# Kernel tuning notes

Hardware: AMD Instinct MI355X
Metric: run time of the kernel (lower is better)

The kernel has to match this reference:

```python
import jax, jax.numpy as jnp
import numpy as np
from math import factorial

LMAX = 2
C_DIM = 128
N = 50000
# (l1, l2, l_out) 'uuu' (channel-wise, no weights) instructions, as in the module ([:3])
INSTR = [(2, 2, 0), (1, 2, 1), (1, 1, 2)]


def _f(n):
    return float(factorial(int(n)))


def _su2_cg(j1, m1, j2, m2, j3, m3):
    # Clebsch-Gordan <j1 m1 j2 m2 | j3 m3> (Racah formula), complex SU(2) basis
    if m3 != m1 + m2:
        return 0.0
    vmin = int(max(-j1 + j2 + m3, -j1 + m1, 0))
    vmax = int(min(j2 + j3 + m1, j3 - j1 + j2, j3 + m3))
    pref = ((2 * j3 + 1) * _f(j3 + j1 - j2) * _f(j3 - j1 + j2) * _f(j1 + j2 - j3) / _f(j1 + j2 + j3 + 1)
            * _f(j3 + m3) * _f(j3 - m3) / (_f(j1 - m1) * _f(j1 + m1) * _f(j2 - m2) * _f(j2 + m2))) ** 0.5
    s = 0.0
    for v in range(vmin, vmax + 1):
        s += (-1.0) ** (v + j2 + m2) / _f(v) * _f(j2 + j3 + m1 - v) * _f(j1 - m1 + v) / (
            _f(j3 - j1 + j2 - v) * _f(j3 + m3 - v) * _f(v + j1 - j2 - m3))
    return pref * s


def _q_real_to_complex(l):
    # e3nn change-of-basis from real to complex spherical harmonics
    q = np.zeros((2 * l + 1, 2 * l + 1), dtype=np.complex128)
    for m in range(-l, 0):
        q[l + m, l + abs(m)] = 1.0 / np.sqrt(2)
        q[l + m, l - abs(m)] = -1j / np.sqrt(2)
    q[l, l] = 1.0
    for m in range(1, l + 1):
        q[l + m, l + abs(m)] = (-1) ** m / np.sqrt(2)
        q[l + m, l - abs(m)] = 1j * (-1) ** m / np.sqrt(2)
    return (-1j) ** l * q


def wigner_3j(l1, l2, l3):
    # real-basis Wigner 3j, unit Frobenius norm (e3nn convention)
    Csu2 = np.zeros((2 * l1 + 1, 2 * l2 + 1, 2 * l3 + 1), dtype=np.complex128)
    for i, m1 in enumerate(range(-l1, l1 + 1)):
        for k, m2 in enumerate(range(-l2, l2 + 1)):
            for n, m3 in enumerate(range(-l3, l3 + 1)):
                Csu2[i, k, n] = _su2_cg(l1, m1, l2, m2, l3, m3)
    Q1, Q2, Q3 = _q_real_to_complex(l1), _q_real_to_complex(l2), _q_real_to_complex(l3)
    C = np.einsum('ij,kl,mn,ikn->jlm', Q1, Q2, np.conj(Q3.T), Csu2)
    assert np.abs(C.imag).max() < 1e-7
    C = C.real
    return (C / np.linalg.norm(C)).astype(np.float32)


W3J = {(l1, l2, lo): jnp.asarray(wigner_3j(l1, l2, lo)) for (l1, l2, lo) in INSTR}


def so3_linear(x, W, b):
    # per-degree block-diagonal linear; x: [N, (LMAX+1)^2, Cin], W: [LMAX+1, Cout, Cin], b: [Cout] (l=0 only)
    outs = []
    for l in range(LMAX + 1):
        y = jnp.einsum('nmc,dc->nmd', x[:, l * l:(l + 1) * (l + 1), :], W[l])
        if l == 0:
            y = y + b
        outs.append(y)
    return jnp.concatenate(outs, axis=1)


def tensor_product_uuu(x1, x2):
    # sparse CG tensor product, channel-shared ('uuu'), no path weights
    out = jnp.zeros_like(x1)
    for (l1, l2, lo) in INSTR:
        w3j = W3J[(l1, l2, lo)]
        alpha = float((2 * lo + 1) ** 0.5)  # component normalization
        blk = alpha * jnp.einsum('ijk,nic,njc->nkc', w3j,
                                 x1[:, l1 * l1:(l1 + 1) ** 2, :],
                                 x2[:, l2 * l2:(l2 + 1) ** 2, :])
        out = out.at[:, lo * lo:(lo + 1) ** 2, :].add(blk)
    return out


def setup_inputs() -> dict:
    key = jax.random.key(0)
    ks = jax.random.split(key, 7)
    scale = 1.0 / np.sqrt(C_DIM)
    m_dim = (LMAX + 1) ** 2  # 9
    return {
        'irreps_x': jax.random.normal(ks[0], (N, m_dim, C_DIM), jnp.float32),
        'W_left': jax.random.normal(ks[1], (LMAX + 1, C_DIM, C_DIM), jnp.float32) * scale,
        'b_left': jax.random.normal(ks[2], (C_DIM,), jnp.float32) * scale,
        'W_right': jax.random.normal(ks[3], (LMAX + 1, C_DIM, C_DIM), jnp.float32) * scale,
        'b_right': jax.random.normal(ks[4], (C_DIM,), jnp.float32) * scale,
        'W_final': jax.random.normal(ks[5], (LMAX + 1, C_DIM, C_DIM), jnp.float32) * scale,
        'b_final': jax.random.normal(ks[6], (C_DIM,), jnp.float32) * scale,
    }


def reference(irreps_x, W_left, b_left, W_right, b_right, W_final, b_final):
    xl = so3_linear(irreps_x, W_left, b_left)
    xr = so3_linear(irreps_x, W_right, b_right)
    out = tensor_product_uuu(xl, xr)
    return so3_linear(out, W_final, b_final)  # [N, 9, C]
```

## Files before the change

kernel.cpp:

```cpp
#include <hip/hip_runtime.h>
#include <cmath>
#include <complex>

typedef unsigned short u16;
typedef unsigned int u32;
typedef __bf16 bf16x8 __attribute__((ext_vector_type(8)));
typedef __bf16 bf16x2 __attribute__((ext_vector_type(2)));
typedef float f32x4 __attribute__((ext_vector_type(4)));
typedef float f32x2 __attribute__((ext_vector_type(2)));

#define CD 128
#define TILE_N 8
#define XS 136
#define LS 132

#define SMEM_TOTAL (72 * XS + 64 * LS + 64 * LS)

struct TPW { float w220[25]; float w121[45]; float w112[45]; };

__device__ __forceinline__ u32 pk2(float a, float b) {
  bf16x2 h;
  h.x = (__bf16)a;
  h.y = (__bf16)b;
  return __builtin_bit_cast(u32, h);
}
__device__ __forceinline__ f32x2 unpk(u32 v) {
  f32x2 r;
  r.x = __uint_as_float(v << 16);
  r.y = __uint_as_float(v & 0xffff0000u);
  return r;
}

__device__ __forceinline__ void ldw4(uint4* dst, const u16* base) {
#pragma unroll
  for (int kk = 0; kk < 4; ++kk)
    dst[kk] = *(const uint4*)(base + kk * 32);
}

__device__ __forceinline__ f32x4 mf(const uint4& a, const uint4& b, f32x4 c) {
  return __builtin_amdgcn_mfma_f32_16x16x32_bf16(
      __builtin_bit_cast(bf16x8, a), __builtin_bit_cast(bf16x8, b), c, 0, 0, 0);
}

__device__ __forceinline__ void stA(u16* d, const f32x4& a) {
  u32 p01 = pk2(a[0], a[1]);
  u32 p23 = pk2(a[2], a[3]);
  d[0]      = (u16)p01;
  d[LS]     = (u16)(p01 >> 16);
  d[2 * LS] = (u16)p23;
  d[3 * LS] = (u16)(p23 >> 16);
}

__global__ void cvt_weights_kernel(const float* __restrict__ Wl,
                                   const float* __restrict__ Wr,
                                   const float* __restrict__ Wf,
                                   u16* __restrict__ ws) {
  int idx = (blockIdx.x * 256 + threadIdx.x) * 8;
  const float* src; int off;
  if (idx < 49152)      { src = Wl; off = idx; }
  else if (idx < 98304) { src = Wr; off = idx - 49152; }
  else                  { src = Wf; off = idx - 98304; }
  float4 a = *(const float4*)(src + off);
  float4 b = *(const float4*)(src + off + 4);
  uint4 v;
  v.x = pk2(a.x, a.y);
  v.y = pk2(a.z, a.w);
  v.z = pk2(b.x, b.y);
  v.w = pk2(b.z, b.w);
  *(uint4*)(ws + idx) = v;
}

__global__ __launch_bounds__(256, 3)
void fused_kernel(const float* __restrict__ x, const u16* __restrict__ ws,
                  const float* __restrict__ bfin, float* __restrict__ out,
                  int N, TPW tw) {
  __shared__ __align__(16) u16 smem[SMEM_TOTAL];
  u16* bufX = smem;
  u16* sTP  = smem;
  u16* sL   = smem + 72 * XS;
  u16* sR   = smem + 72 * XS + 64 * LS;

  const int tid  = threadIdx.x;
  const int n0   = blockIdx.x * TILE_N;
  const int w    = tid >> 6;
  const int lane = tid & 63;
  const int q    = lane >> 4;
  const int lr   = lane & 15;

  const int mat = w >> 1;
  const int wl  = w & 1;
  u16* dstA = mat ? sR : sL;
  const u16* wsA = ws + mat * 3 * 16384;
  const u16* wsf = ws + 6 * 16384;

  const int dc0 = w * 16 + lr;
  const int dc1 = dc0 + 64;
  const float bias0 = bfin[dc0];
  const float bias1 = bfin[dc1];

#pragma unroll
  for (int it = 0; it < 4; ++it) {
    int e = (it * 256 + tid) * 8;
    int r = e >> 7;
    int c = e & 127;
    int n = n0 + (r & 7);
    if (n >= N) n = N - 1;
    int grow = (n * 9 + 1 + (r >> 3)) * CD + c;
    float4 a = *(const float4*)(x + grow);
    float4 b = *(const float4*)(x + grow + 4);
    uint4 v;
    v.x = pk2(a.x, a.y);
    v.y = pk2(a.z, a.w);
    v.z = pk2(b.x, b.y);
    v.w = pk2(b.z, b.w);
    *(uint4*)(bufX + r * XS + c) = v;
  }

  uint4 bfA[4], bfB[4];
  {
    const int colA0 = wl * 64 + lr;
    ldw4(bfA, wsA + 16384 + colA0 * CD + q * 8);
    ldw4(bfB, wsA + 16384 + (colA0 + 16) * CD + q * 8);
  }
  __syncthreads();

#pragma unroll
  for (int p = 0; p < 2; ++p) {
    const int colA = wl * 64 + p * 32 + lr;
    const int colB = colA + 16;
    if (p == 1) {
      ldw4(bfA, wsA + 16384 + colA * CD + q * 8);
      ldw4(bfB, wsA + 16384 + colB * CD + q * 8);
    }
#pragma unroll
    for (int rt = 0; rt < 2; ++rt) {
      const int gbase = rt * 16;
      int ga = gbase + lr; if (ga > 23) ga = 23;
      uint4 av[4];
      ldw4(av, bufX + ga * XS + q * 8);
      f32x4 accA = {0.f, 0.f, 0.f, 0.f};
      f32x4 accB = {0.f, 0.f, 0.f, 0.f};
#pragma unroll
      for (int kk = 0; kk < 4; ++kk) {
        accA = mf(av[kk], bfA[kk], accA);
        accB = mf(av[kk], bfB[kk], accB);
      }
      int g0 = gbase + q * 4;
      if (g0 < 24) {
        stA(dstA + g0 * LS + colA, accA);
        stA(dstA + g0 * LS + colB, accB);
      }
    }
    ldw4(bfA, wsA + 2 * 16384 + colA * CD + q * 8);
    ldw4(bfB, wsA + 2 * 16384 + colB * CD + q * 8);
#pragma unroll
    for (int rt = 0; rt < 3; ++rt) {
      const int gbase = rt * 16;
      int ga = gbase + lr; if (ga > 39) ga = 39;
      uint4 av[4];
      ldw4(av, bufX + (24 + ga) * XS + q * 8);
      f32x4 accA = {0.f, 0.f, 0.f, 0.f};
      f32x4 accB = {0.f, 0.f, 0.f, 0.f};
#pragma unroll
      for (int kk = 0; kk < 4; ++kk) {
        accA = mf(av[kk], bfA[kk], accA);
        accB = mf(av[kk], bfB[kk], accB);
      }
      int g0 = gbase + q * 4;
      if (g0 < 40) {
        stA(dstA + (24 + g0) * LS + colA, accA);
        stA(dstA + (24 + g0) * LS + colB, accB);
      }
    }
  }
  __syncthreads();

#pragma unroll
  for (int iter = 0; iter < 2; ++iter) {
    int id = iter * 256 + tid;
    int cb = (id & 63) * 2;
    int n  = id >> 6;
    const u16* pL = sL + n * LS + cb;
    const u16* pR = sR + n * LS + cb;
    f32x2 xl1[3], xr1[3], xl2[5], xr2[5];
#pragma unroll
    for (int i = 0; i < 3; ++i) {
      xl1[i] = unpk(*(const u32*)(pL + i * 8 * LS));
      xr1[i] = unpk(*(const u32*)(pR + i * 8 * LS));
    }
#pragma unroll
    for (int j = 0; j < 5; ++j) {
      xl2[j] = unpk(*(const u32*)(pL + (24 + j * 8) * LS));
      xr2[j] = unpk(*(const u32*)(pR + (24 + j * 8) * LS));
    }
    f32x2 o0 = {0.f, 0.f};
#pragma unroll
    for (int i = 0; i < 5; ++i) {
      f32x2 t = {0.f, 0.f};
#pragma unroll
      for (int j = 0; j < 5; ++j) t += tw.w220[i * 5 + j] * xr2[j];
      o0 += xl2[i] * t;
    }
    f32x2 o1[3] = {{0.f,0.f},{0.f,0.f},{0.f,0.f}};
#pragma unroll
    for (int i = 0; i < 3; ++i)
#pragma unroll
      for (int j = 0; j < 5; ++j) {
        f32x2 pr = xl1[i] * xr2[j];
#pragma unroll
        for (int k = 0; k < 3; ++k) o1[k] += tw.w121[(i * 5 + j) * 3 + k] * pr;
      }
    f32x2 o2[5] = {{0.f,0.f},{0.f,0.f},{0.f,0.f},{0.f,0.f},{0.f,0.f}};
#pragma unroll
    for (int i = 0; i < 3; ++i)
#pragma unroll
      for (int j = 0; j < 3; ++j) {
        f32x2 pr = xl1[i] * xr1[j];
#pragma unroll
        for (int k = 0; k < 5; ++k) o2[k] += tw.w112[(i * 3 + j) * 5 + k] * pr;
      }
    u16* pT = sTP + n * XS + cb;
    *(u32*)(pT) = pk2(o0.x, o0.y);
#pragma unroll
    for (int k = 0; k < 3; ++k) *(u32*)(pT + (1 + k) * 8 * XS) = pk2(o1[k].x, o1[k].y);
#pragma unroll
    for (int k = 0; k < 5; ++k) *(u32*)(pT + (4 + k) * 8 * XS) = pk2(o2[k].x, o2[k].y);
  }

  uint4 bc0[4], bc1[4];
  ldw4(bc0, wsf + dc0 * CD + q * 8);
  ldw4(bc1, wsf + dc1 * CD + q * 8);
  __syncthreads();

#pragma unroll
  for (int l = 0; l < 3; ++l) {
    if (l > 0) {
      ldw4(bc0, wsf + l * 16384 + dc0 * CD + q * 8);
      ldw4(bc1, wsf + l * 16384 + dc1 * CD + q * 8);
    }
    const int rows   = (l == 0) ? 8 : (l == 1 ? 24 : 40);
    const int soff   = (l == 0) ? 0 : (l == 1 ? 8 : 32);
    const int ntl    = (l == 0) ? 1 : (l == 1 ? 2 : 3);
#pragma unroll
    for (int t = 0; t < 3; ++t) {
      if (t >= ntl) continue;
      int ga = t * 16 + lr; if (ga > rows - 1) ga = rows - 1;
      uint4 av[4];
      ldw4(av, sTP + (soff + ga) * XS + q * 8);
      f32x4 a0 = {0.f, 0.f, 0.f, 0.f};
      f32x4 a1 = {0.f, 0.f, 0.f, 0.f};
#pragma unroll
      for (int kk = 0; kk < 4; ++kk) {
        a0 = mf(av[kk], bc0[kk], a0);
        a1 = mf(av[kk], bc1[kk], a1);
      }
#pragma unroll
      for (int reg = 0; reg < 4; ++reg) {
        int gg = t * 16 + q * 4 + reg;
        if (gg < rows) {
          int m = l * l + (gg >> 3);
          int n = n0 + (gg & 7);
          if (n < N) {
            float v0 = a0[reg], v1 = a1[reg];
            if (l == 0) { v0 += bias0; v1 += bias1; }
            out[(n * 9 + m) * CD + dc0] = v0;
            out[(n * 9 + m) * CD + dc1] = v1;
          }
        }
      }
    }
  }
}

typedef std::complex<double> cd;

static double factd(int n) { double r = 1.0; for (int i = 2; i <= n; ++i) r *= i; return r; }

static double su2_cg(int j1, int m1, int j2, int m2, int j3, int m3) {
  if (m3 != m1 + m2) return 0.0;
  int vmin = -j1 + j2 + m3; if (-j1 + m1 > vmin) vmin = -j1 + m1; if (0 > vmin) vmin = 0;
  int vmax = j2 + j3 + m1; if (j3 - j1 + j2 < vmax) vmax = j3 - j1 + j2; if (j3 + m3 < vmax) vmax = j3 + m3;
  double pref = std::sqrt((2.0 * j3 + 1.0) * factd(j3 + j1 - j2) * factd(j3 - j1 + j2)
                          * factd(j1 + j2 - j3) / factd(j1 + j2 + j3 + 1)
                          * factd(j3 + m3) * factd(j3 - m3)
                          / (factd(j1 - m1) * factd(j1 + m1) * factd(j2 - m2) * factd(j2 + m2)));
  double s = 0.0;
  for (int v = vmin; v <= vmax; ++v) {
    double sgn = ((v + j2 + m2) & 1) ? -1.0 : 1.0;
    s += sgn / factd(v) * factd(j2 + j3 + m1 - v) * factd(j1 - m1 + v)
         / (factd(j3 - j1 + j2 - v) * factd(j3 + m3 - v) * factd(v + j1 - j2 - m3));
  }
  return pref * s;
}

static void qmat(int l, cd q[5][5]) {
  for (int a = 0; a < 5; ++a) for (int b = 0; b < 5; ++b) q[a][b] = 0.0;
  const double is2 = 1.0 / std::sqrt(2.0);
  for (int m = -l; m < 0; ++m) {
    q[l + m][l - m] = is2;
    q[l + m][l + m] = cd(0.0, -is2);
  }
  q[l][l] = 1.0;
  for (int m = 1; m <= l; ++m) {
    double s = (m & 1) ? -1.0 : 1.0;
    q[l + m][l + m] = s * is2;
    q[l + m][l - m] = cd(0.0, s * is2);
  }
  cd f(1.0, 0.0);
  for (int i = 0; i < l; ++i) f *= cd(0.0, -1.0);
  for (int a = 0; a < 5; ++a) for (int b = 0; b < 5; ++b) q[a][b] *= f;
}

static void wigner3j(int l1, int l2, int l3, double* C) {
  int d1 = 2 * l1 + 1, d2 = 2 * l2 + 1, d3 = 2 * l3 + 1;
  cd Q1[5][5], Q2[5][5], Q3[5][5];
  qmat(l1, Q1); qmat(l2, Q2); qmat(l3, Q3);
  cd Csu2[5][5][5];
  for (int i = 0; i < d1; ++i)
    for (int k = 0; k < d2; ++k)
      for (int n = 0; n < d3; ++n)
        Csu2[i][k][n] = su2_cg(l1, i - l1, l2, k - l2, l3, n - l3);
  double norm = 0.0;
  for (int j = 0; j < d1; ++j)
    for (int lx = 0; lx < d2; ++lx)
      for (int m = 0; m < d3; ++m) {
        cd acc(0.0, 0.0);
        for (int i = 0; i < d1; ++i)
          for (int k = 0; k < d2; ++k)
            for (int n = 0; n < d3; ++n)
              acc += Q1[i][j] * Q2[k][lx] * std::conj(Q3[n][m]) * Csu2[i][k][n];
        C[(j * d2 + lx) * d3 + m] = acc.real();
        norm += acc.real() * acc.real();
      }
  norm = std::sqrt(norm);
  for (int t = 0; t < d1 * d2 * d3; ++t) C[t] /= norm;
}

extern "C" void kernel_launch(void* const* d_in, const int* in_sizes, int n_in,
                              void* d_out, int out_size, void* d_ws, size_t ws_size,
                              hipStream_t stream) {
  const float* x    = (const float*)d_in[0];
  const float* Wl   = (const float*)d_in[1];
  const float* Wr   = (const float*)d_in[3];
  const float* Wf   = (const float*)d_in[5];
  const float* bfin = (const float*)d_in[6];
  float* out = (float*)d_out;
  const int N = in_sizes[0] / (9 * CD);

  TPW tw;
  double c220[25], c121[45], c112[45];
  wigner3j(2, 2, 0, c220);
  wigner3j(1, 2, 1, c121);
  wigner3j(1, 1, 2, c112);
  const double a1 = std::sqrt(3.0), a2 = std::sqrt(5.0);
  for (int i = 0; i < 25; ++i) tw.w220[i] = (float)c220[i];
  for (int i = 0; i < 45; ++i) tw.w121[i] = (float)(a1 * c121[i]);
  for (int i = 0; i < 45; ++i) tw.w112[i] = (float)(a2 * c112[i]);

  u16* ws = (u16*)d_ws;
  cvt_weights_kernel<<<72, 256, 0, stream>>>(Wl, Wr, Wf, ws);
  int grid = (N + TILE_N - 1) / TILE_N;
  fused_kernel<<<grid, 256, 0, stream>>>(x, ws, bfin, out, N, tw);
}
```

Measured before the change: 495.7 us.

## Transpose left/right activation smem to channel-major and widen GEMM column tiles

```diff
diff --git a/kernel.cpp b/kernel.cpp
--- a/kernel.cpp
+++ b/kernel.cpp
@@ -12,9 +12,9 @@
 #define CD 128
 #define TILE_N 8
 #define XS 136
-#define LS 132
-
-#define SMEM_TOTAL (72 * XS + 64 * LS + 64 * LS)
+#define CS 66
+
+#define SMEM_TOTAL (72 * XS + 2 * 128 * CS)
 
 struct TPW { float w220[25]; float w121[45]; float w112[45]; };
 
@@ -43,12 +43,9 @@
 }
 
 __device__ __forceinline__ void stA(u16* d, const f32x4& a) {
-  u32 p01 = pk2(a[0], a[1]);
-  u32 p23 = pk2(a[2], a[3]);
-  d[0]      = (u16)p01;
-  d[LS]     = (u16)(p01 >> 16);
-  d[2 * LS] = (u16)p23;
-  d[3 * LS] = (u16)(p23 >> 16);
+  u32* p = (u32*)d;
+  p[0] = pk2(a[0], a[1]);
+  p[1] = pk2(a[2], a[3]);
 }
 
 __global__ void cvt_weights_kernel(const float* __restrict__ Wl,
@@ -78,7 +75,7 @@
   u16* bufX = smem;
   u16* sTP  = smem;
   u16* sL   = smem + 72 * XS;
-  u16* sR   = smem + 72 * XS + 64 * LS;
+  u16* sR   = sL + 128 * CS;
 
   const int tid  = threadIdx.x;
   const int n0   = blockIdx.x * TILE_N;
@@ -116,61 +113,62 @@
     *(uint4*)(bufX + r * XS + c) = v;
   }
 
-  uint4 bfA[4], bfB[4];
-  {
-    const int colA0 = wl * 64 + lr;
-    ldw4(bfA, wsA + 16384 + colA0 * CD + q * 8);
-    ldw4(bfB, wsA + 16384 + (colA0 + 16) * CD + q * 8);
-  }
+  const int colb = wl * 64 + lr;
+  uint4 wf0[4], wf1[4], wf2[4], wf3[4];
+  ldw4(wf0, wsA + 16384 + (colb     ) * CD + q * 8);
+  ldw4(wf1, wsA + 16384 + (colb + 16) * CD + q * 8);
+  ldw4(wf2, wsA + 16384 + (colb + 32) * CD + q * 8);
+  ldw4(wf3, wsA + 16384 + (colb + 48) * CD + q * 8);
   __syncthreads();
 
 #pragma unroll
-  for (int p = 0; p < 2; ++p) {
-    const int colA = wl * 64 + p * 32 + lr;
-    const int colB = colA + 16;
-    if (p == 1) {
-      ldw4(bfA, wsA + 16384 + colA * CD + q * 8);
-      ldw4(bfB, wsA + 16384 + colB * CD + q * 8);
-    }
-#pragma unroll
-    for (int rt = 0; rt < 2; ++rt) {
-      const int gbase = rt * 16;
-      int ga = gbase + lr; if (ga > 23) ga = 23;
-      uint4 av[4];
-      ldw4(av, bufX + ga * XS + q * 8);
-      f32x4 accA = {0.f, 0.f, 0.f, 0.f};
-      f32x4 accB = {0.f, 0.f, 0.f, 0.f};
-#pragma unroll
-      for (int kk = 0; kk < 4; ++kk) {
-        accA = mf(av[kk], bfA[kk], accA);
-        accB = mf(av[kk], bfB[kk], accB);
-      }
-      int g0 = gbase + q * 4;
-      if (g0 < 24) {
-        stA(dstA + g0 * LS + colA, accA);
-        stA(dstA + g0 * LS + colB, accB);
-      }
-    }
-    ldw4(bfA, wsA + 2 * 16384 + colA * CD + q * 8);
-    ldw4(bfB, wsA + 2 * 16384 + colB * CD + q * 8);
-#pragma unroll
-    for (int rt = 0; rt < 3; ++rt) {
-      const int gbase = rt * 16;
-      int ga = gbase + lr; if (ga > 39) ga = 39;
-      uint4 av[4];
-      ldw4(av, bufX + (24 + ga) * XS + q * 8);
-      f32x4 accA = {0.f, 0.f, 0.f, 0.f};
-      f32x4 accB = {0.f, 0.f, 0.f, 0.f};
-#pragma unroll
-      for (int kk = 0; kk < 4; ++kk) {
-        accA = mf(av[kk], bfA[kk], accA);
-        accB = mf(av[kk], bfB[kk], accB);
-      }
-      int g0 = gbase + q * 4;
-      if (g0 < 40) {
-        stA(dstA + (24 + g0) * LS + colA, accA);
-        stA(dstA + (24 + g0) * LS + colB, accB);
-      }
+  for (int rt = 0; rt < 2; ++rt) {
+    const int gbase = rt * 16;
+    int ga = gbase + lr; if (ga > 23) ga = 23;
+    uint4 av[4];
+    ldw4(av, bufX + ga * XS + q * 8);
+    f32x4 a0 = {0.f,0.f,0.f,0.f}, a1 = {0.f,0.f,0.f,0.f};
+    f32x4 a2 = {0.f,0.f,0.f,0.f}, a3 = {0.f,0.f,0.f,0.f};
+#pragma unroll
+    for (int kk = 0; kk < 4; ++kk) {
+      a0 = mf(av[kk], wf0[kk], a0);
+      a1 = mf(av[kk], wf1[kk], a1);
+      a2 = mf(av[kk], wf2[kk], a2);
+      a3 = mf(av[kk], wf3[kk], a3);
+    }
+    int g0 = gbase + q * 4;
+    if (g0 < 24) {
+      stA(dstA + (colb     ) * CS + g0, a0);
+      stA(dstA + (colb + 16) * CS + g0, a1);
+      stA(dstA + (colb + 32) * CS + g0, a2);
+      stA(dstA + (colb + 48) * CS + g0, a3);
+    }
+  }
+  ldw4(wf0, wsA + 2 * 16384 + (colb     ) * CD + q * 8);
+  ldw4(wf1, wsA + 2 * 16384 + (colb + 16) * CD + q * 8);
+  ldw4(wf2, wsA + 2 * 16384 + (colb + 32) * CD + q * 8);
+  ldw4(wf3, wsA + 2 * 16384 + (colb + 48) * CD + q * 8);
+#pragma unroll
+  for (int rt = 0; rt < 3; ++rt) {
+    const int gbase = rt * 16;
+    int ga = gbase + lr; if (ga > 39) ga = 39;
+    uint4 av[4];
+    ldw4(av, bufX + (24 + ga) * XS + q * 8);
+    f32x4 a0 = {0.f,0.f,0.f,0.f}, a1 = {0.f,0.f,0.f,0.f};
+    f32x4 a2 = {0.f,0.f,0.f,0.f}, a3 = {0.f,0.f,0.f,0.f};
+#pragma unroll
+    for (int kk = 0; kk < 4; ++kk) {
+      a0 = mf(av[kk], wf0[kk], a0);
+      a1 = mf(av[kk], wf1[kk], a1);
+      a2 = mf(av[kk], wf2[kk], a2);
+      a3 = mf(av[kk], wf3[kk], a3);
+    }
+    int g0 = gbase + q * 4;
+    if (g0 < 40) {
+      stA(dstA + (colb     ) * CS + 24 + g0, a0);
+      stA(dstA + (colb + 16) * CS + 24 + g0, a1);
+      stA(dstA + (colb + 32) * CS + 24 + g0, a2);
+      stA(dstA + (colb + 48) * CS + 24 + g0, a3);
     }
   }
   __syncthreads();
@@ -178,20 +176,20 @@
 #pragma unroll
   for (int iter = 0; iter < 2; ++iter) {
     int id = iter * 256 + tid;
-    int cb = (id & 63) * 2;
-    int n  = id >> 6;
-    const u16* pL = sL + n * LS + cb;
-    const u16* pR = sR + n * LS + cb;
+    int ch = id & 127;
+    int n  = (id >> 7) * 2;
+    const u16* pL = sL + ch * CS + n;
+    const u16* pR = sR + ch * CS + n;
     f32x2 xl1[3], xr1[3], xl2[5], xr2[5];
 #pragma unroll
     for (int i = 0; i < 3; ++i) {
-      xl1[i] = unpk(*(const u32*)(pL + i * 8 * LS));
-      xr1[i] = unpk(*(const u32*)(pR + i * 8 * LS));
+      xl1[i] = unpk(*(const u32*)(pL + i * 8));
+      xr1[i] = unpk(*(const u32*)(pR + i * 8));
     }
 #pragma unroll
     for (int j = 0; j < 5; ++j) {
-      xl2[j] = unpk(*(const u32*)(pL + (24 + j * 8) * LS));
-      xr2[j] = unpk(*(const u32*)(pR + (24 + j * 8) * LS));
+      xl2[j] = unpk(*(const u32*)(pL + 24 + j * 8));
+      xr2[j] = unpk(*(const u32*)(pR + 24 + j * 8));
     }
     f32x2 o0 = {0.f, 0.f};
 #pragma unroll
@@ -219,12 +217,24 @@
 #pragma unroll
         for (int k = 0; k < 5; ++k) o2[k] += tw.w112[(i * 3 + j) * 5 + k] * pr;
       }
-    u16* pT = sTP + n * XS + cb;
-    *(u32*)(pT) = pk2(o0.x, o0.y);
-#pragma unroll
-    for (int k = 0; k < 3; ++k) *(u32*)(pT + (1 + k) * 8 * XS) = pk2(o1[k].x, o1[k].y);
-#pragma unroll
-    for (int k = 0; k < 5; ++k) *(u32*)(pT + (4 + k) * 8 * XS) = pk2(o2[k].x, o2[k].y);
+    u16* pT = sTP + n * XS + ch;
+    u32 v0 = pk2(o0.x, o0.y);
+    pT[0]  = (u16)v0;
+    pT[XS] = (u16)(v0 >> 16);
+#pragma unroll
+    for (int k = 0; k < 3; ++k) {
+      u32 v = pk2(o1[k].x, o1[k].y);
+      u16* b = pT + (1 + k) * 8 * XS;
+      b[0]  = (u16)v;
+      b[XS] = (u16)(v >> 16);
+    }
+#pragma unroll
+    for (int k = 0; k < 5; ++k) {
+      u32 v = pk2(o2[k].x, o2[k].y);
+      u16* b = pT + (4 + k) * 8 * XS;
+      b[0]  = (u16)v;
+      b[XS] = (u16)(v >> 16);
+    }
   }
 
   uint4 bc0[4], bc1[4];
```

New measurement: 493.9 us. No clear change (-0.4%).
